# Kernel tuning notes

Measured on AMD Instinct MI355X. Metric: run time of the kernel, lower is better.

## Reference

```python
import jax, jax.numpy as jnp
import numpy as np

H = 1024  # hidden size

def _lstm_cell(x, h, c, Wih, Whh, bih, bhh):
    # gates: [B, 4H], torch LSTMCell layout i|f|g|o
    gates = x @ Wih.T + bih + h @ Whh.T + bhh
    i, f, g, o = jnp.split(gates, 4, axis=-1)
    i = jax.nn.sigmoid(i)
    f = jax.nn.sigmoid(f)
    g = jnp.tanh(g)
    o = jax.nn.sigmoid(o)
    c_new = f * c + i * g
    h_new = o * jnp.tanh(c_new)
    return h_new, c_new


def setup_inputs() -> dict:
    key = jax.random.key(0)
    ks = jax.random.split(key, 11)
    B, T = 512, 256
    s_in = 1.0 / np.sqrt(2.0)
    s_h = 1.0 / np.sqrt(H)
    return {
        "x": jax.random.normal(ks[0], (B, T, 2), jnp.float32),
        "Wih0": jax.random.normal(ks[1], (4 * H, 2), jnp.float32) * s_in,
        "Whh0": jax.random.normal(ks[2], (4 * H, H), jnp.float32) * s_h,
        "bih0": jnp.full((4 * H,), 0.01, jnp.float32),
        "bhh0": jnp.full((4 * H,), 0.01, jnp.float32),
        "Wih1": jax.random.normal(ks[3], (4 * H, H), jnp.float32) * s_h,
        "Whh1": jax.random.normal(ks[4], (4 * H, H), jnp.float32) * s_h,
        "bih1": jnp.full((4 * H,), 0.01, jnp.float32),
        "bhh1": jnp.full((4 * H,), 0.01, jnp.float32),
        "Wl": jax.random.normal(ks[5], (1, H), jnp.float32) * s_h,
        "bl": jnp.full((1,), 0.01, jnp.float32),
        "future_pred": 0,
    }


def reference(x, Wih0, Whh0, bih0, bhh0, Wih1, Whh1, bih1, bhh1, Wl, bl, future_pred):
    # output into an input-size-2 LSTMCell, which would error in torch.
    assert future_pred == 0
    B = x.shape[0]
    h0 = jnp.zeros((B, H), jnp.float32)
    zeros = (h0, h0, h0, h0)  # h0, c0, h1, c1

    def step(carry, xt):
        h0, c0, h1, c1 = carry
        h0, c0 = _lstm_cell(xt, h0, c0, Wih0, Whh0, bih0, bhh0)
        h1, c1 = _lstm_cell(h0, h1, c1, Wih1, Whh1, bih1, bhh1)
        y = h1 @ Wl.T + bl  # [B, 1]
        return (h0, c0, h1, c1), y

    xs = jnp.swapaxes(x, 0, 1)  # [T, B, 2]
    _, ys = jax.lax.scan(step, zeros, xs)  # ys: [T, B, 1]
    return jnp.swapaxes(ys[..., 0], 0, 1)  # [B, T]
```

## Files before the change

### kernel.cpp

```cpp
#include <hip/hip_runtime.h>
#include <hip/hip_bf16.h>


#define B_   512
#define T_   256
#define H_   1024
#define BM   128
#define BH   16
#define BNG  64
#define BK   64
#define PAD  8
#define LDK  (BK + PAD)
#define WSZ  4194304L
#define HBSZ 524288L

#define WHI_SCALE   512.0f
#define WLO_SCALE   1048576.0f
#define HLO_SCALE   2048.0f
#define ACCH_DESC   (1.0f / 512.0f)
#define ACCL_DESC   (1.0f / 1048576.0f)

typedef _Float16 f16;
typedef _Float16 half8 __attribute__((ext_vector_type(8)));
typedef float f32x4 __attribute__((ext_vector_type(4)));

__device__ __forceinline__ float sigmoidf_fast(float x) {
  return 1.0f / (1.0f + __builtin_exp2f(-1.44269504f * x));
}
__device__ __forceinline__ float tanhf_fast(float x) {
  float ax = __builtin_fabsf(x);
  float e = __builtin_exp2f(-2.88539008f * ax);
  float t = (1.0f - e) / (1.0f + e);
  return __builtin_copysignf(t, x);
}

__global__ void prep_kernel(const float* __restrict__ Whh0, const float* __restrict__ Wih1,
                            const float* __restrict__ Whh1,
                            const float* __restrict__ bih0, const float* __restrict__ bhh0,
                            const float* __restrict__ bih1, const float* __restrict__ bhh1,
                            const float* __restrict__ bl,
                            f16* __restrict__ Whh0h, f16* __restrict__ Wih1h, f16* __restrict__ Whh1h,
                            float* __restrict__ b0s, float* __restrict__ b1s,
                            f16* __restrict__ h0a, f16* __restrict__ h1a,
                            float* __restrict__ c0, float* __restrict__ c1,
                            float* __restrict__ y)
{
  const long W = WSZ, HB = HBSZ;
  const long total = 3 * W + 8192 + 4 * HB + 2 * HB + 131072;
  long idx = (long)blockIdx.x * 256 + threadIdx.x;
  long stride = (long)gridDim.x * 256;
  for (long i = idx; i < total; i += stride) {
    long r = i;
    if (r < 3 * W) {
      const float* src; f16* dst;
      if (r < W)          { src = Whh0; dst = Whh0h; }
      else if (r < 2 * W) { src = Wih1; dst = Wih1h; r -= W; }
      else                { src = Whh1; dst = Whh1h; r -= 2 * W; }
      float w = src[r];
      f16 hi = (f16)w;
      float hif = (float)hi;
      dst[r]     = (f16)(hif * WHI_SCALE);
      dst[W + r] = (f16)((w - hif) * WLO_SCALE);
      continue;
    }
    r -= 3 * W;
    if (r < 4096) { b0s[r] = bih0[r] + bhh0[r]; continue; } r -= 4096;
    if (r < 4096) { b1s[r] = bih1[r] + bhh1[r]; continue; } r -= 4096;
    if (r < 2 * HB) { h0a[r] = (f16)0.0f; continue; } r -= 2 * HB;
    if (r < 2 * HB) { h1a[r] = (f16)0.0f; continue; } r -= 2 * HB;
    if (r < HB) { c0[r] = 0.0f; continue; } r -= HB;
    if (r < HB) { c1[r] = 0.0f; continue; } r -= HB;
    y[r] = bl[0];
  }
}

__launch_bounds__(256, 2)
__global__ void step_kernel(int t,
    const float* __restrict__ x,
    const float* __restrict__ Wih0,
    const float* __restrict__ Wl,
    const f16* __restrict__ Whh0h,
    const f16* __restrict__ Wih1h,
    const f16* __restrict__ Whh1h,
    const float* __restrict__ b0s, const float* __restrict__ b1s,
    f16* __restrict__ h0a, f16* __restrict__ h0b,
    f16* __restrict__ h1a, f16* __restrict__ h1b,
    float* __restrict__ c0, float* __restrict__ c1,
    float* __restrict__ y)
{
  __shared__ f16 At[2][BM][LDK];
  __shared__ f16 Bt[2][BNG][LDK];

  const int bid = blockIdx.x;
  const int tid = threadIdx.x;
  const bool l1 = bid >= 256;
  const int lb = bid & 255;
  const int mt = lb >> 6;
  const int hs = lb & 63;
  const int r0 = mt * BM;
  const int j0 = hs * BH;

  const f16 *hA, *hB = nullptr;
  const f16 *WA, *WB = nullptr;
  f16* hout; float* cc;
  int tt, NK;
  if (!l1) {
    if (t >= T_) return;
    tt = t;
    hA   = (t & 1) ? h0b : h0a;
    hout = (t & 1) ? h0a : h0b;
    WA = Whh0h;
    cc = c0; NK = H_ / BK;
  } else {
    if (t == 0) return;
    tt = t - 1;
    hA   = ((tt + 1) & 1) ? h0b : h0a;
    hB   = (tt & 1) ? h1b : h1a;
    hout = ((tt + 1) & 1) ? h1b : h1a;
    WA = Wih1h; WB = Whh1h;
    cc = c1; NK = 2 * H_ / BK;
  }

  const int lane = tid & 63;
  const int wv = tid >> 6;
  const int sr = tid >> 3;
  const int sc = tid & 7;

  f32x4 accH[2][4] = {};
  f32x4 accL[2][4] = {};
  f32x4 ar[8];
  f32x4 br[4];

  auto stage_load = [&](int ki) {
    const f16* hsrc; const f16* wsrc; int ko;
    if (!l1 || ki < 16) { hsrc = hA; wsrc = WA; ko = ki * BK; }
    else                { hsrc = hB; wsrc = WB; ko = (ki - 16) * BK; }
    #pragma unroll
    for (int i = 0; i < 4; i++) {
      int row = sr + 32 * i;
      long off = (long)(r0 + row) * H_ + ko + sc * 8;
      ar[i]     = *(const f32x4*)&hsrc[off];
      ar[4 + i] = *(const f32x4*)&hsrc[HBSZ + off];
    }
    #pragma unroll
    for (int i = 0; i < 2; i++) {
      int row = sr + 32 * i;
      long off = (long)((row >> 4) * H_ + j0 + (row & 15)) * H_ + ko + sc * 8;
      br[i]     = *(const f32x4*)&wsrc[off];
      br[2 + i] = *(const f32x4*)&wsrc[WSZ + off];
    }
  };
  auto stage_store = [&]() {
    #pragma unroll
    for (int i = 0; i < 4; i++) {
      int row = sr + 32 * i;
      *(f32x4*)&At[0][row][sc * 8] = ar[i];
      *(f32x4*)&At[1][row][sc * 8] = ar[4 + i];
    }
    #pragma unroll
    for (int i = 0; i < 2; i++) {
      int row = sr + 32 * i;
      *(f32x4*)&Bt[0][row][sc * 8] = br[i];
      *(f32x4*)&Bt[1][row][sc * 8] = br[2 + i];
    }
  };
  auto do_compute = [&]() {
    const int arow = wv * 32 + (lane & 15);
    const int bcol = lane & 15;
    const int kq = (lane >> 4) * 8;
    #pragma unroll
    for (int kk = 0; kk < 2; kk++) {
      half8 ah[2], al[2], bh[4], bl_[4];
      #pragma unroll
      for (int mi = 0; mi < 2; mi++) {
        ah[mi] = *(const half8*)&At[0][arow + mi * 16][kk * 32 + kq];
        al[mi] = *(const half8*)&At[1][arow + mi * 16][kk * 32 + kq];
      }
      #pragma unroll
      for (int ni = 0; ni < 4; ni++) {
        bh[ni]  = *(const half8*)&Bt[0][ni * 16 + bcol][kk * 32 + kq];
        bl_[ni] = *(const half8*)&Bt[1][ni * 16 + bcol][kk * 32 + kq];
      }
      #pragma unroll
      for (int mi = 0; mi < 2; mi++)
        #pragma unroll
        for (int ni = 0; ni < 4; ni++) {
          accH[mi][ni] = __builtin_amdgcn_mfma_f32_16x16x32_f16(ah[mi], bh[ni],  accH[mi][ni], 0, 0, 0);
          accL[mi][ni] = __builtin_amdgcn_mfma_f32_16x16x32_f16(ah[mi], bl_[ni], accL[mi][ni], 0, 0, 0);
          accL[mi][ni] = __builtin_amdgcn_mfma_f32_16x16x32_f16(al[mi], bh[ni],  accL[mi][ni], 0, 0, 0);
        }
    }
  };

  stage_load(0);
  for (int ki = 0; ki < NK; ki++) {
    __syncthreads();
    stage_store();
    __syncthreads();
    if (ki + 1 < NK) stage_load(ki + 1);
    do_compute();
  }

  const int j = j0 + (lane & 15);
  const float* bs = l1 ? b1s : b0s;
  float bsum[4], wi0[4][2];
  #pragma unroll
  for (int g = 0; g < 4; g++) bsum[g] = bs[g * H_ + j];
  if (!l1) {
    #pragma unroll
    for (int g = 0; g < 4; g++) {
      wi0[g][0] = Wih0[(g * H_ + j) * 2 + 0];
      wi0[g][1] = Wih0[(g * H_ + j) * 2 + 1];
    }
  }
  const float wl = l1 ? Wl[j] : 0.0f;

  #pragma unroll
  for (int mi = 0; mi < 2; mi++) {
    #pragma unroll
    for (int r = 0; r < 4; r++) {
      int row = r0 + wv * 32 + mi * 16 + ((lane >> 4) & 3) * 4 + r;
      float gi = accH[mi][0][r] * ACCH_DESC + accL[mi][0][r] * ACCL_DESC + bsum[0];
      float gf = accH[mi][1][r] * ACCH_DESC + accL[mi][1][r] * ACCL_DESC + bsum[1];
      float gg = accH[mi][2][r] * ACCH_DESC + accL[mi][2][r] * ACCL_DESC + bsum[2];
      float go = accH[mi][3][r] * ACCH_DESC + accL[mi][3][r] * ACCL_DESC + bsum[3];
      if (!l1) {
        float x0 = x[(row * T_ + tt) * 2 + 0];
        float x1 = x[(row * T_ + tt) * 2 + 1];
        gi += x0 * wi0[0][0] + x1 * wi0[0][1];
        gf += x0 * wi0[1][0] + x1 * wi0[1][1];
        gg += x0 * wi0[2][0] + x1 * wi0[2][1];
        go += x0 * wi0[3][0] + x1 * wi0[3][1];
      }
      float ig = sigmoidf_fast(gi);
      float fg = sigmoidf_fast(gf);
      float gv = tanhf_fast(gg);
      float ov = sigmoidf_fast(go);
      int cidx = row * H_ + j;
      float cn = fg * cc[cidx] + ig * gv;
      cc[cidx] = cn;
      float hn = ov * tanhf_fast(cn);
      f16 hhi = (f16)hn;
      hout[cidx] = hhi;
      hout[cidx + HBSZ] = (f16)((hn - (float)hhi) * HLO_SCALE);
      if (l1) {
        float yp = hn * wl;
        #pragma unroll
        for (int s = 1; s < 16; s <<= 1) yp += __shfl_xor(yp, s, 64);
        if ((lane & 15) == 0) atomicAdd(&y[row * T_ + tt], yp);
      }
    }
  }
}

extern "C" void kernel_launch(void* const* d_in, const int* in_sizes, int n_in,
                              void* d_out, int out_size, void* d_ws, size_t ws_size,
                              hipStream_t stream) {
  (void)in_sizes; (void)n_in; (void)out_size; (void)ws_size;
  const float* x    = (const float*)d_in[0];
  const float* Wih0 = (const float*)d_in[1];
  const float* Whh0 = (const float*)d_in[2];
  const float* bih0 = (const float*)d_in[3];
  const float* bhh0 = (const float*)d_in[4];
  const float* Wih1 = (const float*)d_in[5];
  const float* Whh1 = (const float*)d_in[6];
  const float* bih1 = (const float*)d_in[7];
  const float* bhh1 = (const float*)d_in[8];
  const float* Wl   = (const float*)d_in[9];
  const float* bl   = (const float*)d_in[10];
  float* y = (float*)d_out;

  char* ws = (char*)d_ws;
  size_t off = 0;
  auto alloc = [&](size_t bytes) { char* p = ws + off; off += (bytes + 255) & ~255UL; return p; };
  f16*   Whh0h = (f16*)alloc(2 * WSZ * sizeof(f16));
  f16*   Wih1h = (f16*)alloc(2 * WSZ * sizeof(f16));
  f16*   Whh1h = (f16*)alloc(2 * WSZ * sizeof(f16));
  float* b0s   = (float*)alloc(4096 * sizeof(float));
  float* b1s   = (float*)alloc(4096 * sizeof(float));
  f16*   h0a   = (f16*)alloc(2 * HBSZ * sizeof(f16));
  f16*   h0b   = (f16*)alloc(2 * HBSZ * sizeof(f16));
  f16*   h1a   = (f16*)alloc(2 * HBSZ * sizeof(f16));
  f16*   h1b   = (f16*)alloc(2 * HBSZ * sizeof(f16));
  float* c0    = (float*)alloc(HBSZ * sizeof(float));
  float* c1    = (float*)alloc(HBSZ * sizeof(float));

  hipLaunchKernelGGL(prep_kernel, dim3(2048), dim3(256), 0, stream,
      Whh0, Wih1, Whh1, bih0, bhh0, bih1, bhh1, bl,
      Whh0h, Wih1h, Whh1h, b0s, b1s, h0a, h1a, c0, c1, y);

  for (int t = 0; t <= T_; t++) {
    hipLaunchKernelGGL(step_kernel, dim3(512), dim3(256), 0, stream, t,
        x, Wih0, Wl, Whh0h, Wih1h, Whh1h, b0s, b1s,
        h0a, h0b, h1a, h1b, c0, c1, y);
  }
}
```

Baseline: 14.54 ms.

## Enlarge per-block tile and stream tiles into LDS with async global_load_lds

Each block now computes 128 rows by 32 hidden units (128 gate columns) with a 2x2 wave layout, halving the grid to 256 blocks. Operand tiles go straight from global memory to XOR-swizzled LDS through global_load_lds, double-buffered with one barrier per k-step instead of staging through registers. The aim is more reuse of each loaded tile and less register and barrier overhead. In exchange, fewer blocks run per step (256 on a GPU with many CUs), occupancy drops to one block per SIMD set, and the swizzle and plane-interleaving indexing become more complex.

```diff
diff --git a/kernel.cpp b/kernel.cpp
--- a/kernel.cpp
+++ b/kernel.cpp
@@ -6,11 +6,8 @@
 #define T_   256
 #define H_   1024
 #define BM   128
-#define BH   16
-#define BNG  64
-#define BK   64
-#define PAD  8
-#define LDK  (BK + PAD)
+#define BH   32
+#define BK   32
 #define WSZ  4194304L
 #define HBSZ 524288L
 
@@ -74,7 +71,7 @@
   }
 }
 
-__launch_bounds__(256, 2)
+__launch_bounds__(256, 1)
 __global__ void step_kernel(int t,
     const float* __restrict__ x,
     const float* __restrict__ Wih0,
@@ -88,15 +85,14 @@
     float* __restrict__ c0, float* __restrict__ c1,
     float* __restrict__ y)
 {
-  __shared__ f16 At[2][BM][LDK];
-  __shared__ f16 Bt[2][BNG][LDK];
+  __shared__ __align__(16) char smem[2][2][128][128];
 
   const int bid = blockIdx.x;
   const int tid = threadIdx.x;
-  const bool l1 = bid >= 256;
-  const int lb = bid & 255;
-  const int mt = lb >> 6;
-  const int hs = lb & 63;
+  const bool l1 = bid >= 128;
+  const int lb = l1 ? bid - 128 : bid;
+  const int mt = lb >> 5;
+  const int hs = lb & 31;
   const int r0 = mt * BM;
   const int j0 = hs * BH;
 
@@ -123,85 +119,89 @@
 
   const int lane = tid & 63;
   const int wv = tid >> 6;
-  const int sr = tid >> 3;
-  const int sc = tid & 7;
-
-  f32x4 accH[2][4] = {};
-  f32x4 accL[2][4] = {};
-  f32x4 ar[8];
-  f32x4 br[4];
-
-  auto stage_load = [&](int ki) {
-    const f16* hsrc; const f16* wsrc; int ko;
-    if (!l1 || ki < 16) { hsrc = hA; wsrc = WA; ko = ki * BK; }
-    else                { hsrc = hB; wsrc = WB; ko = (ki - 16) * BK; }
-    #pragma unroll
-    for (int i = 0; i < 4; i++) {
-      int row = sr + 32 * i;
-      long off = (long)(r0 + row) * H_ + ko + sc * 8;
-      ar[i]     = *(const f32x4*)&hsrc[off];
-      ar[4 + i] = *(const f32x4*)&hsrc[HBSZ + off];
-    }
-    #pragma unroll
-    for (int i = 0; i < 2; i++) {
-      int row = sr + 32 * i;
-      long off = (long)((row >> 4) * H_ + j0 + (row & 15)) * H_ + ko + sc * 8;
-      br[i]     = *(const f32x4*)&wsrc[off];
-      br[2 + i] = *(const f32x4*)&wsrc[WSZ + off];
+  const int wvm = wv >> 1;
+  const int wvn = wv & 1;
+  const int ln15 = lane & 15;
+
+  const int rsub  = lane >> 3;
+  const int ubl   = (lane & 7) << 4;
+  const int ubs   = ubl ^ (rsub << 4);
+  const int spl   = ubs >> 6;
+  const int skb   = ubs & 63;
+
+  f32x4 accH[4][4] = {};
+  f32x4 accL[4][4] = {};
+
+  auto stage = [&](int ki, int buf) {
+    const f16* hsrc; const f16* wsrc; long ko2;
+    if (!l1 || ki < 32) { hsrc = hA; wsrc = WA; ko2 = (long)ki * BK * 2; }
+    else                { hsrc = hB; wsrc = WB; ko2 = (long)(ki - 32) * BK * 2; }
+    const long aPl = spl ? HBSZ * 2 : 0;
+    const long bPl = spl ? WSZ * 2 : 0;
+    #pragma unroll
+    for (int n = 0; n < 8; n++) {
+      const int c = wv * 8 + n;
+      long gbyte; const char* srcb; char* dst;
+      if (c < 16) {
+        int row = c * 8 + rsub;
+        gbyte = aPl + (long)(r0 + row) * 2048 + ko2 + skb;
+        srcb = (const char*)hsrc;
+        dst = &smem[buf][0][c * 8][0];
+      } else {
+        int row = (c - 16) * 8 + rsub;
+        int gate = (row >> 4) & 3, sub = row >> 6;
+        int wrow = gate * H_ + j0 + sub * 16 + (row & 15);
+        gbyte = bPl + (long)wrow * 2048 + ko2 + skb;
+        srcb = (const char*)wsrc;
+        dst = &smem[buf][1][(c - 16) * 8][0];
+      }
+      __builtin_amdgcn_global_load_lds(
+          (const __attribute__((address_space(1))) void*)(srcb + gbyte),
+          (__attribute__((address_space(3))) void*)dst, 16, 0, 0);
     }
   };
-  auto stage_store = [&]() {
-    #pragma unroll
-    for (int i = 0; i < 4; i++) {
-      int row = sr + 32 * i;
-      *(f32x4*)&At[0][row][sc * 8] = ar[i];
-      *(f32x4*)&At[1][row][sc * 8] = ar[4 + i];
-    }
-    #pragma unroll
-    for (int i = 0; i < 2; i++) {
-      int row = sr + 32 * i;
-      *(f32x4*)&Bt[0][row][sc * 8] = br[i];
-      *(f32x4*)&Bt[1][row][sc * 8] = br[2 + i];
-    }
-  };
-  auto do_compute = [&]() {
-    const int arow = wv * 32 + (lane & 15);
-    const int bcol = lane & 15;
-    const int kq = (lane >> 4) * 8;
-    #pragma unroll
-    for (int kk = 0; kk < 2; kk++) {
-      half8 ah[2], al[2], bh[4], bl_[4];
-      #pragma unroll
-      for (int mi = 0; mi < 2; mi++) {
-        ah[mi] = *(const half8*)&At[0][arow + mi * 16][kk * 32 + kq];
-        al[mi] = *(const half8*)&At[1][arow + mi * 16][kk * 32 + kq];
-      }
+
+  const int kqb = (lane >> 4) << 4;
+  const int swz = (ln15 & 7) << 4;
+  const int uhi = kqb ^ swz;
+  const int ulo = (64 | kqb) ^ swz;
+
+  auto compute = [&](int buf) {
+    const char* base = &smem[buf][0][0][0];
+    half8 ah[4], al[4], bh[4], blo[4];
+    #pragma unroll
+    for (int mi = 0; mi < 4; mi++) {
+      int row = wvm * 64 + mi * 16 + ln15;
+      ah[mi] = *(const half8*)(base + row * 128 + uhi);
+      al[mi] = *(const half8*)(base + row * 128 + ulo);
+    }
+    #pragma unroll
+    for (int ni = 0; ni < 4; ni++) {
+      int row = wvn * 64 + ni * 16 + ln15;
+      bh[ni]  = *(const half8*)(base + 16384 + row * 128 + uhi);
+      blo[ni] = *(const half8*)(base + 16384 + row * 128 + ulo);
+    }
+    #pragma unroll
+    for (int mi = 0; mi < 4; mi++)
       #pragma unroll
       for (int ni = 0; ni < 4; ni++) {
-        bh[ni]  = *(const half8*)&Bt[0][ni * 16 + bcol][kk * 32 + kq];
-        bl_[ni] = *(const half8*)&Bt[1][ni * 16 + bcol][kk * 32 + kq];
-      }
-      #pragma unroll
-      for (int mi = 0; mi < 2; mi++)
-        #pragma unroll
-        for (int ni = 0; ni < 4; ni++) {
-          accH[mi][ni] = __builtin_amdgcn_mfma_f32_16x16x32_f16(ah[mi], bh[ni],  accH[mi][ni], 0, 0, 0);
-          accL[mi][ni] = __builtin_amdgcn_mfma_f32_16x16x32_f16(ah[mi], bl_[ni], accL[mi][ni], 0, 0, 0);
-          accL[mi][ni] = __builtin_amdgcn_mfma_f32_16x16x32_f16(al[mi], bh[ni],  accL[mi][ni], 0, 0, 0);
-        }
-    }
+        accH[mi][ni] = __builtin_amdgcn_mfma_f32_16x16x32_f16(ah[mi], bh[ni],  accH[mi][ni], 0, 0, 0);
+        accL[mi][ni] = __builtin_amdgcn_mfma_f32_16x16x32_f16(ah[mi], blo[ni], accL[mi][ni], 0, 0, 0);
+        accL[mi][ni] = __builtin_amdgcn_mfma_f32_16x16x32_f16(al[mi], bh[ni],  accL[mi][ni], 0, 0, 0);
+      }
   };
 
-  stage_load(0);
+  stage(0, 0);
+  __syncthreads();
+  int buf = 0;
   for (int ki = 0; ki < NK; ki++) {
+    if (ki + 1 < NK) stage(ki + 1, buf ^ 1);
+    compute(buf);
     __syncthreads();
-    stage_store();
-    __syncthreads();
-    if (ki + 1 < NK) stage_load(ki + 1);
-    do_compute();
-  }
-
-  const int j = j0 + (lane & 15);
+    buf ^= 1;
+  }
+
+  const int j = j0 + wvn * 16 + ln15;
   const float* bs = l1 ? b1s : b0s;
   float bsum[4], wi0[4][2];
   #pragma unroll
@@ -214,12 +214,13 @@
     }
   }
   const float wl = l1 ? Wl[j] : 0.0f;
+  const int grp = (lane >> 4) & 3;
 
   #pragma unroll
-  for (int mi = 0; mi < 2; mi++) {
+  for (int mi = 0; mi < 4; mi++) {
     #pragma unroll
     for (int r = 0; r < 4; r++) {
-      int row = r0 + wv * 32 + mi * 16 + ((lane >> 4) & 3) * 4 + r;
+      int row = r0 + wvm * 64 + mi * 16 + grp * 4 + r;
       float gi = accH[mi][0][r] * ACCH_DESC + accL[mi][0][r] * ACCL_DESC + bsum[0];
       float gf = accH[mi][1][r] * ACCH_DESC + accL[mi][1][r] * ACCL_DESC + bsum[1];
       float gg = accH[mi][2][r] * ACCH_DESC + accL[mi][2][r] * ACCL_DESC + bsum[2];
@@ -247,7 +248,7 @@
         float yp = hn * wl;
         #pragma unroll
         for (int s = 1; s < 16; s <<= 1) yp += __shfl_xor(yp, s, 64);
-        if ((lane & 15) == 0) atomicAdd(&y[row * T_ + tt], yp);
+        if (ln15 == 0) atomicAdd(&y[row * T_ + tt], yp);
       }
     }
   }
@@ -290,7 +291,7 @@
       Whh0h, Wih1h, Whh1h, b0s, b1s, h0a, h1a, c0, c1, y);
 
   for (int t = 0; t <= T_; t++) {
-    hipLaunchKernelGGL(step_kernel, dim3(512), dim3(256), 0, stream, t,
+    hipLaunchKernelGGL(step_kernel, dim3(256), dim3(256), 0, stream, t,
         x, Wih0, Wl, Whh0h, Wih1h, Whh1h, b0s, b1s,
         h0a, h0b, h1a, h1b, c0, c1, y);
   }
```

Measured after the change: 18.88 ms. 1.3x slower.
